# Optimization experiments

Measured on AMD Instinct MI355X. Metric: run time of the kernel, lower is better.

Reference implementation:

```python
import jax, jax.numpy as jnp
import numpy as np

T = 3000
D_MODEL = 1280
NUM_HEADS = 20
HEAD_DIM = D_MODEL // NUM_HEADS
N_CHUNKS = 4  # block-diagonal chunks of 750 frames each
NEG = -1e9


def _block_diag_mask(t, n_chunks):
    chunk = t // n_chunks
    seg = jnp.arange(t) // chunk  # [T]
    allow = seg[:, None] == seg[None, :]
    return jnp.where(allow, 0.0, NEG).astype(jnp.float32)


def setup_inputs() -> dict:
    key = jax.random.key(0)
    ks = jax.random.split(key, 9)
    s = 1.0 / np.sqrt(D_MODEL)
    inp = {
        "hidden_states": jax.random.normal(ks[0], (T, D_MODEL), jnp.float32),
        "attention_mask": _block_diag_mask(T, N_CHUNKS),
        "wq": jax.random.normal(ks[1], (D_MODEL, D_MODEL), jnp.float32) * s,
        "bq": jax.random.normal(ks[2], (D_MODEL,), jnp.float32) * 0.02,
        "wk": jax.random.normal(ks[3], (D_MODEL, D_MODEL), jnp.float32) * s,
        "bk": jax.random.normal(ks[4], (D_MODEL,), jnp.float32) * 0.02,
        "wv": jax.random.normal(ks[5], (D_MODEL, D_MODEL), jnp.float32) * s,
        "bv": jax.random.normal(ks[6], (D_MODEL,), jnp.float32) * 0.02,
        "wo": jax.random.normal(ks[7], (D_MODEL, D_MODEL), jnp.float32) * s,
        "bo": jax.random.normal(ks[8], (D_MODEL,), jnp.float32) * 0.02,
    }
    return inp


def reference(hidden_states, attention_mask, wq, bq, wk, bk, wv, bv, wo, bo):
    # hidden_states: [T, D], attention_mask: [T, T] additive (0 / -inf)
    t = hidden_states.shape[0]
    scaling = HEAD_DIM ** -0.5
    # projections -> [H, T, hd]  (weights stored as [in, out] = W^T of nn.Linear)
    q = (hidden_states @ wq + bq).reshape(t, NUM_HEADS, HEAD_DIM).transpose(1, 0, 2)
    k = (hidden_states @ wk + bk).reshape(t, NUM_HEADS, HEAD_DIM).transpose(1, 0, 2)
    v = (hidden_states @ wv + bv).reshape(t, NUM_HEADS, HEAD_DIM).transpose(1, 0, 2)
    # [H, T, T] scores + additive mask, fp32 softmax
    scores = jnp.einsum("htd,hsd->hts", q, k) * scaling + attention_mask[None]
    attn = jax.nn.softmax(scores.astype(jnp.float32), axis=-1).astype(q.dtype)
    out = jnp.einsum("hts,hsd->htd", attn, v)  # [H, T, hd]
    out = out.transpose(1, 0, 2).reshape(t, D_MODEL)
    return out @ wo + bo
```

## Files before the change

kernel.cpp:

```cpp
#include <hip/hip_runtime.h>

#define T_LEN 3000
#define DM 1280
#define NUM_HEADS 20
#define N_CH 4
#define CHUNK 750
#define CHUNK_PAD 768
#define T_PAD 3072

typedef __bf16 bf16x8 __attribute__((ext_vector_type(8)));
typedef float f32x4 __attribute__((ext_vector_type(4)));

typedef const __attribute__((address_space(1))) void* gas_p;
typedef __attribute__((address_space(3))) void* las_p;
#define GLOAD16(g, l) __builtin_amdgcn_global_load_lds((gas_p)(g), (las_p)(l), 16, 0, 0)

__device__ __forceinline__ unsigned short f2bf(float f) {
  union { float f; unsigned u; } x; x.f = f;
  unsigned r = x.u + 0x7FFFu + ((x.u >> 16) & 1u);
  return (unsigned short)(r >> 16);
}

__global__ __launch_bounds__(256) void cvt_bf16_kernel(
    const float* __restrict__ in, unsigned short* __restrict__ out) {
  int i = blockIdx.x * 256 + threadIdx.x;
  ushort4 o;
  if (i < T_LEN * DM / 4) {
    const float4 v = ((const float4*)in)[i];
    o.x = f2bf(v.x); o.y = f2bf(v.y); o.z = f2bf(v.z); o.w = f2bf(v.w);
  } else {
    o.x = 0; o.y = 0; o.z = 0; o.w = 0;
  }
  ((ushort4*)out)[i] = o;
}

__global__ __launch_bounds__(256) void tr_bf16_kernel(
    const float* __restrict__ w0, const float* __restrict__ w1,
    const float* __restrict__ w2, const float* __restrict__ w3,
    unsigned short* __restrict__ out) {
  const int z = blockIdx.z;
  const float* in = z == 0 ? w0 : (z == 1 ? w1 : (z == 2 ? w2 : w3));
  unsigned short* o = out + (size_t)z * DM * DM;
  __shared__ float tile[32][33];
  const int x = threadIdx.x, y0 = threadIdx.y;
  const int n0 = blockIdx.x * 32, k0 = blockIdx.y * 32;
  for (int y = y0; y < 32; y += 8) tile[y][x] = in[(k0 + y) * DM + n0 + x];
  __syncthreads();
  for (int y = y0; y < 32; y += 8) o[(n0 + y) * DM + k0 + x] = f2bf(tile[x][y]);
}

__global__ __launch_bounds__(256) void vpad_zero_kernel(unsigned short* __restrict__ Vtb) {
  int i = blockIdx.x * 256 + threadIdx.x;
  if (i >= NUM_HEADS * 64 * N_CH * (CHUNK_PAD - CHUNK)) return;
  int c = i % (CHUNK_PAD - CHUNK); int r = i / (CHUNK_PAD - CHUNK);
  int ch = r % N_CH; int row = r / N_CH;
  Vtb[(size_t)row * T_PAD + ch * CHUNK_PAD + CHUNK + c] = 0;
}

template <int MODE>
__global__ __launch_bounds__(256) void gemm_kernel(
    const unsigned short* __restrict__ A, const unsigned short* __restrict__ Bt,
    const float* __restrict__ b0, const float* __restrict__ b1, const float* __restrict__ b2,
    unsigned short* __restrict__ dq, unsigned short* __restrict__ dk,
    unsigned short* __restrict__ dv, float* __restrict__ df) {
  __shared__ unsigned short As[128][64];
  __shared__ unsigned short Bs[64][64];
  const int tid = threadIdx.x;
  const int lane = tid & 63, wave = tid >> 6;
  const int h = lane >> 4, lr = lane & 15;
  const int wm = wave >> 1, wn = wave & 1;
  const int t0 = blockIdx.x * 128, n0 = blockIdx.y * 64;
  const int rs = lane >> 3;
  const int c8 = (lane & 7) ^ rs;

  const unsigned short* Ab = A + (size_t)t0 * DM + c8 * 8;
  const unsigned short* Bb = Bt + (size_t)n0 * DM + c8 * 8;

  f32x4 acc[4][2];
  const f32x4 zero4 = {0.f, 0.f, 0.f, 0.f};
#pragma unroll
  for (int i = 0; i < 4; i++)
#pragma unroll
    for (int j = 0; j < 2; j++) acc[i][j] = zero4;

  const int NT = DM / 64;
  for (int kt = 0; kt < NT; ++kt) {
    const int k0 = kt * 64;
#pragma unroll
    for (int i = 0; i < 4; ++i) {
      const int blk = wave * 4 + i;
      GLOAD16(Ab + (size_t)(blk * 8 + rs) * DM + k0, &As[blk * 8][0]);
    }
#pragma unroll
    for (int i = 0; i < 2; ++i) {
      const int blk = wave * 2 + i;
      GLOAD16(Bb + (size_t)(blk * 8 + rs) * DM + k0, &Bs[blk * 8][0]);
    }
    __syncthreads();
#pragma unroll
    for (int kk = 0; kk < 2; ++kk) {
      bf16x8 a[4], b[2];
      const int csw = ((kk * 4 + h) ^ (lr & 7)) * 8;
#pragma unroll
      for (int mi = 0; mi < 4; mi++) a[mi] = *(const bf16x8*)&As[wm * 64 + mi * 16 + lr][csw];
#pragma unroll
      for (int ni = 0; ni < 2; ni++) b[ni] = *(const bf16x8*)&Bs[wn * 32 + ni * 16 + lr][csw];
#pragma unroll
      for (int mi = 0; mi < 4; mi++)
#pragma unroll
        for (int ni = 0; ni < 2; ni++)
          acc[mi][ni] = __builtin_amdgcn_mfma_f32_16x16x32_bf16(a[mi], b[ni], acc[mi][ni], 0, 0, 0);
    }
    __syncthreads();
  }

  const int sec = (MODE == 0) ? ((int)blockIdx.y / 20) : 0;
  const float* bias = (MODE == 0) ? (sec == 0 ? b0 : (sec == 1 ? b1 : b2)) : b0;
  const float qs = (MODE == 0 && sec == 0) ? 0.125f : 1.0f;
#pragma unroll
  for (int mi = 0; mi < 4; mi++) {
#pragma unroll
    for (int j = 0; j < 4; j++) {
      int t = t0 + wm * 64 + mi * 16 + h * 4 + j;
      if (t >= T_LEN) continue;
#pragma unroll
      for (int ni = 0; ni < 2; ni++) {
        int n = n0 + wn * 32 + ni * 16 + lr;
        if (MODE == 0) {
          int nn = n - sec * DM;
          float v = (acc[mi][ni][j] + bias[nn]) * qs;
          if (sec < 2) {
            unsigned short* dst = sec == 0 ? dq : dk;
            dst[(size_t)(nn >> 6) * (T_PAD * 64) + (size_t)t * 64 + (nn & 63)] = f2bf(v);
          } else {
            int ch = t / CHUNK, s = t - ch * CHUNK;
            dv[(size_t)(nn >> 6) * (64 * T_PAD) + (size_t)(nn & 63) * T_PAD + ch * CHUNK_PAD + s] = f2bf(v);
          }
        } else {
          df[(size_t)t * DM + n] = acc[mi][ni][j] + bias[n];
        }
      }
    }
  }
}

__global__ __launch_bounds__(256) void attn_kernel(
    const unsigned short* __restrict__ Qb, const unsigned short* __restrict__ Kb,
    const unsigned short* __restrict__ Vtb, unsigned short* __restrict__ Ctx) {
  __shared__ unsigned short Ks[2][64][64];
  __shared__ unsigned short Vs[2][64][64];
  __shared__ unsigned short Ps[4][16][64];
  const int tid = threadIdx.x;
  const int lane = tid & 63, wave = tid >> 6;
  const int h = lane >> 4, lr = lane & 15;
  const int rs = lane >> 3;
  const int c8 = (lane & 7) ^ rs;
  int bid = blockIdx.x;
  const int qt = bid % 12; bid /= 12;
  const int ch = bid % N_CH; bid /= N_CH;
  const int hh = bid;

  const unsigned short* Qh = Qb + (size_t)hh * (T_PAD * 64);
  const unsigned short* Kh = Kb + (size_t)hh * (T_PAD * 64) + (size_t)(ch * CHUNK) * 64 + c8 * 8;
  const unsigned short* Vh = Vtb + (size_t)hh * (64 * T_PAD) + ch * CHUNK_PAD + c8 * 8;

  const int qrow0 = qt * 64 + wave * 16;
  const int tq = ch * CHUNK + qrow0 + lr;
  bf16x8 aq[2];
#pragma unroll
  for (int kk = 0; kk < 2; kk++)
    aq[kk] = *(const bf16x8*)(Qh + (size_t)tq * 64 + kk * 32 + h * 8);

  const f32x4 zero4 = {0.f, 0.f, 0.f, 0.f};
  f32x4 oacc[4];
#pragma unroll
  for (int i = 0; i < 4; i++) oacc[i] = zero4;
  float l_part[4] = {0.f, 0.f, 0.f, 0.f};

#define A_STAGE(buf, kt) do {                                                   \
    const int s0_ = (kt) * 64;                                                  \
    _Pragma("unroll")                                                           \
    for (int i_ = 0; i_ < 2; ++i_) {                                            \
      const int blk_ = wave * 2 + i_;                                           \
      const int r_ = blk_ * 8 + rs;                                             \
      GLOAD16(Kh + (size_t)(s0_ + r_) * 64, &Ks[buf][blk_ * 8][0]);             \
      GLOAD16(Vh + (size_t)r_ * T_PAD + s0_, &Vs[buf][blk_ * 8][0]);            \
    } } while (0)

  A_STAGE(0, 0);
  __syncthreads();
  int cur = 0;
  for (int kt = 0; kt < 12; ++kt) {
    if (kt + 1 < 12) A_STAGE(cur ^ 1, kt + 1);

    f32x4 sacc[4];
#pragma unroll
    for (int i = 0; i < 4; i++) sacc[i] = zero4;
#pragma unroll
    for (int kk = 0; kk < 2; kk++) {
      const int csw = ((kk * 4 + h) ^ (lr & 7)) * 8;
      bf16x8 bk[4];
#pragma unroll
      for (int ni = 0; ni < 4; ni++) bk[ni] = *(const bf16x8*)&Ks[cur][ni * 16 + lr][csw];
#pragma unroll
      for (int ni = 0; ni < 4; ni++)
        sacc[ni] = __builtin_amdgcn_mfma_f32_16x16x32_bf16(aq[kk], bk[ni], sacc[ni], 0, 0, 0);
    }

    const bool last = (kt == 11);
    float pexp[4][4];
#pragma unroll
    for (int ni = 0; ni < 4; ni++) {
#pragma unroll
      for (int j = 0; j < 4; j++) {
        float e = __expf(sacc[ni][j]);
        if (last && (ni * 16 + lr >= CHUNK - 704)) e = 0.f;
        pexp[ni][j] = e;
        l_part[j] += e;
      }
    }

#pragma unroll
    for (int ni = 0; ni < 4; ni++) {
#pragma unroll
      for (int j = 0; j < 4; j++) {
        int row = h * 4 + j;
        int col = ni * 16 + lr;
        Ps[wave][row][((col >> 3) ^ (row & 7)) * 8 + (col & 7)] = f2bf(pexp[ni][j]);
      }
    }

#pragma unroll
    for (int kk = 0; kk < 2; kk++) {
      const int csw = ((kk * 4 + h) ^ (lr & 7)) * 8;
      bf16x8 ap = *(const bf16x8*)&Ps[wave][lr][csw];
      bf16x8 bv[4];
#pragma unroll
      for (int nd = 0; nd < 4; nd++) bv[nd] = *(const bf16x8*)&Vs[cur][nd * 16 + lr][csw];
#pragma unroll
      for (int nd = 0; nd < 4; nd++)
        oacc[nd] = __builtin_amdgcn_mfma_f32_16x16x32_bf16(ap, bv[nd], oacc[nd], 0, 0, 0);
    }
    __syncthreads();
    cur ^= 1;
  }
#undef A_STAGE

#pragma unroll
  for (int j = 0; j < 4; j++) {
    float l = l_part[j];
#pragma unroll
    for (int off = 1; off < 16; off <<= 1) l += __shfl_xor(l, off, 64);
    int qr = qrow0 + h * 4 + j;
    if (qr >= CHUNK) continue;
    int t = ch * CHUNK + qr;
    float inv = 1.f / l;
#pragma unroll
    for (int nd = 0; nd < 4; nd++) {
      int d = nd * 16 + lr;
      Ctx[(size_t)t * DM + hh * 64 + d] = f2bf(oacc[nd][j] * inv);
    }
  }
}

extern "C" void kernel_launch(void* const* d_in, const int* in_sizes, int n_in,
                              void* d_out, int out_size, void* d_ws, size_t ws_size,
                              hipStream_t stream) {
  const float* hs = (const float*)d_in[0];
  const float* wq = (const float*)d_in[2];
  const float* bq = (const float*)d_in[3];
  const float* wk = (const float*)d_in[4];
  const float* bk = (const float*)d_in[5];
  const float* wv = (const float*)d_in[6];
  const float* bv = (const float*)d_in[7];
  const float* wo = (const float*)d_in[8];
  const float* bo = (const float*)d_in[9];

  char* ws = (char*)d_ws;
  unsigned short* Xb = (unsigned short*)ws;   ws += (size_t)T_PAD * DM * 2;
  unsigned short* Wcat = (unsigned short*)ws; ws += (size_t)4 * DM * DM * 2;
  unsigned short* Qb = (unsigned short*)ws;   ws += (size_t)NUM_HEADS * T_PAD * 64 * 2;
  unsigned short* Kb = (unsigned short*)ws;   ws += (size_t)NUM_HEADS * T_PAD * 64 * 2;
  unsigned short* Vtb = (unsigned short*)ws;  ws += (size_t)NUM_HEADS * 64 * T_PAD * 2;
  unsigned short* Ctx = (unsigned short*)ws;  ws += (size_t)T_PAD * DM * 2;

  cvt_bf16_kernel<<<T_PAD * DM / 4 / 256, 256, 0, stream>>>(hs, Xb);
  tr_bf16_kernel<<<dim3(40, 40, 4), dim3(32, 8), 0, stream>>>(wq, wk, wv, wo, Wcat);
  vpad_zero_kernel<<<(NUM_HEADS * 64 * N_CH * (CHUNK_PAD - CHUNK) + 255) / 256, 256, 0, stream>>>(Vtb);

  gemm_kernel<0><<<dim3(24, 60), 256, 0, stream>>>(Xb, Wcat, bq, bk, bv, Qb, Kb, Vtb, nullptr);

  attn_kernel<<<NUM_HEADS * N_CH * 12, 256, 0, stream>>>(Qb, Kb, Vtb, Ctx);

  gemm_kernel<1><<<dim3(24, 20), 256, 0, stream>>>(Ctx, Wcat + (size_t)3 * DM * DM, bo, nullptr, nullptr,
                                                   nullptr, nullptr, nullptr, (float*)d_out);
}
```

Baseline: 129.3 us.

## Use 256x256 double-buffered pipelined GEMM for fused QKV projection

Replaces the 128x64-tile QKV projection GEMM with a dedicated 512-thread kernel using 256x256 tiles. It double-buffers LDS with async global-to-LDS loads interleaved across eight compute phases, and raises MFMA wave priority while computing. The aim is more operand reuse per byte loaded and overlap of memory traffic with matrix math. The trade-off is only 180 blocks (fewer than the CU count), 128 KB of LDS per block, and heavy register use from 32 accumulators. The output projection keeps the old kernel, split into its own non-templated version.

```diff
diff --git a/kernel.cpp b/kernel.cpp
--- a/kernel.cpp
+++ b/kernel.cpp
@@ -57,12 +57,128 @@
   Vtb[(size_t)row * T_PAD + ch * CHUNK_PAD + CHUNK + c] = 0;
 }
 
-template <int MODE>
-__global__ __launch_bounds__(256) void gemm_kernel(
+__global__ __launch_bounds__(512, 2) void gemm256_kernel(
     const unsigned short* __restrict__ A, const unsigned short* __restrict__ Bt,
     const float* __restrict__ b0, const float* __restrict__ b1, const float* __restrict__ b2,
     unsigned short* __restrict__ dq, unsigned short* __restrict__ dk,
-    unsigned short* __restrict__ dv, float* __restrict__ df) {
+    unsigned short* __restrict__ dv) {
+  __shared__ unsigned short Asd[2][256][64];
+  __shared__ unsigned short Bsd[2][256][64];
+  const int tid = threadIdx.x;
+  const int lane = tid & 63, wave = tid >> 6;
+  const int h = lane >> 4, lr = lane & 15;
+  const int wm = wave >> 2, wn = wave & 3;
+  const int t0 = blockIdx.x * 256, n0 = blockIdx.y * 256;
+
+  const int r8 = lane >> 3;
+  const int sg = (lane & 7) ^ r8;
+  const unsigned short* Ast = A + (size_t)(t0 + wave * 8 + r8) * DM + sg * 8;
+  const unsigned short* Bst = Bt + (size_t)(n0 + wave * 8 + r8) * DM + sg * 8;
+
+#define STG_A(BUF, HALF, KT) do {                                                        \
+    GLOAD16(Ast + (size_t)((HALF) * 128) * DM + (size_t)(KT) * 64,                       \
+            &Asd[BUF][(HALF) * 128 + wave * 8][0]);                                      \
+    GLOAD16(Ast + (size_t)((HALF) * 128 + 64) * DM + (size_t)(KT) * 64,                  \
+            &Asd[BUF][(HALF) * 128 + 64 + wave * 8][0]);                                 \
+  } while (0)
+#define STG_B(BUF, HALF, KT) do {                                                        \
+    GLOAD16(Bst + (size_t)((HALF) * 128) * DM + (size_t)(KT) * 64,                       \
+            &Bsd[BUF][(HALF) * 128 + wave * 8][0]);                                      \
+    GLOAD16(Bst + (size_t)((HALF) * 128 + 64) * DM + (size_t)(KT) * 64,                  \
+            &Bsd[BUF][(HALF) * 128 + 64 + wave * 8][0]);                                 \
+  } while (0)
+
+  f32x4 acc[8][4];
+  const f32x4 zero4 = {0.f, 0.f, 0.f, 0.f};
+#pragma unroll
+  for (int i = 0; i < 8; i++)
+#pragma unroll
+    for (int j = 0; j < 4; j++) acc[i][j] = zero4;
+
+#define PHASE(BUF, MH, NH, STAGE_STMT, GATE_STMT) do {                                   \
+    bf16x8 pa[4][2], pb[2][2];                                                           \
+    _Pragma("unroll") for (int mf = 0; mf < 4; mf++)                                     \
+      _Pragma("unroll") for (int kk = 0; kk < 2; kk++) {                                 \
+        const int R = (MH) * 128 + wm * 64 + mf * 16 + lr;                               \
+        pa[mf][kk] = *(const bf16x8*)&Asd[BUF][R][((kk * 4 + h) ^ (lr & 7)) * 8];        \
+      }                                                                                  \
+    _Pragma("unroll") for (int nf = 0; nf < 2; nf++)                                     \
+      _Pragma("unroll") for (int kk = 0; kk < 2; kk++) {                                 \
+        const int Cc = (NH) * 128 + wn * 32 + nf * 16 + lr;                              \
+        pb[nf][kk] = *(const bf16x8*)&Bsd[BUF][Cc][((kk * 4 + h) ^ (lr & 7)) * 8];       \
+      }                                                                                  \
+    STAGE_STMT;                                                                          \
+    __builtin_amdgcn_s_barrier();                                                        \
+    __builtin_amdgcn_s_setprio(1);                                                       \
+    _Pragma("unroll") for (int mf = 0; mf < 4; mf++)                                     \
+      _Pragma("unroll") for (int nf = 0; nf < 2; nf++)                                   \
+        _Pragma("unroll") for (int kk = 0; kk < 2; kk++)                                 \
+          acc[(MH) * 4 + mf][(NH) * 2 + nf] = __builtin_amdgcn_mfma_f32_16x16x32_bf16(   \
+              pa[mf][kk], pb[nf][kk], acc[(MH) * 4 + mf][(NH) * 2 + nf], 0, 0, 0);       \
+    __builtin_amdgcn_s_setprio(0);                                                       \
+    GATE_STMT;                                                                           \
+    __builtin_amdgcn_s_barrier();                                                        \
+  } while (0)
+
+  STG_A(0, 0, 0); STG_B(0, 0, 0); STG_A(0, 1, 0); STG_B(0, 1, 0);
+  STG_A(1, 0, 1); STG_B(1, 0, 1);
+  asm volatile("s_waitcnt vmcnt(4)" ::: "memory");
+  __builtin_amdgcn_s_barrier();
+
+#pragma unroll 1
+  for (int i = 0; i < 10; ++i) {
+    const int tA = 2 * i, tB = 2 * i + 1;
+    PHASE(0, 0, 0, STG_A(1, 1, tB), );
+    PHASE(0, 0, 1, STG_B(1, 1, tB), );
+    PHASE(0, 1, 0, if (i < 9) STG_A(0, 0, tA + 2), );
+    PHASE(0, 1, 1, if (i < 9) STG_B(0, 0, tA + 2),
+          if (i < 9) { asm volatile("s_waitcnt vmcnt(4)" ::: "memory"); }
+          else       { asm volatile("s_waitcnt vmcnt(0)" ::: "memory"); });
+    PHASE(1, 0, 0, if (i < 9) STG_A(0, 1, tA + 2), );
+    PHASE(1, 0, 1, if (i < 9) STG_B(0, 1, tA + 2), );
+    PHASE(1, 1, 0, if (i < 9) STG_A(1, 0, tB + 2), );
+    PHASE(1, 1, 1, if (i < 9) STG_B(1, 0, tB + 2),
+          if (i < 9) { asm volatile("s_waitcnt vmcnt(4)" ::: "memory"); });
+  }
+#undef PHASE
+#undef STG_A
+#undef STG_B
+
+  const int sec = (int)blockIdx.y / 5;
+  const float* bias = sec == 0 ? b0 : (sec == 1 ? b1 : b2);
+  const float qs = sec == 0 ? 0.125f : 1.0f;
+#pragma unroll
+  for (int mh = 0; mh < 2; mh++) {
+#pragma unroll
+    for (int mf = 0; mf < 4; mf++) {
+#pragma unroll
+      for (int jj = 0; jj < 4; jj++) {
+        int t = t0 + mh * 128 + wm * 64 + mf * 16 + h * 4 + jj;
+        if (t >= T_LEN) continue;
+#pragma unroll
+        for (int nh = 0; nh < 2; nh++) {
+#pragma unroll
+          for (int nf = 0; nf < 2; nf++) {
+            int n = n0 + nh * 128 + wn * 32 + nf * 16 + lr;
+            int nn = n - sec * DM;
+            float v = (acc[mh * 4 + mf][nh * 2 + nf][jj] + bias[nn]) * qs;
+            if (sec < 2) {
+              unsigned short* dst = sec == 0 ? dq : dk;
+              dst[(size_t)(nn >> 6) * (T_PAD * 64) + (size_t)t * 64 + (nn & 63)] = f2bf(v);
+            } else {
+              int ch = t / CHUNK, s = t - ch * CHUNK;
+              dv[(size_t)(nn >> 6) * (64 * T_PAD) + (size_t)(nn & 63) * T_PAD + ch * CHUNK_PAD + s] = f2bf(v);
+            }
+          }
+        }
+      }
+    }
+  }
+}
+
+__global__ __launch_bounds__(256) void gemm_out_kernel(
+    const unsigned short* __restrict__ A, const unsigned short* __restrict__ Bt,
+    const float* __restrict__ b0, float* __restrict__ df) {
   __shared__ unsigned short As[128][64];
   __shared__ unsigned short Bs[64][64];
   const int tid = threadIdx.x;
@@ -114,9 +230,6 @@
     __syncthreads();
   }
 
-  const int sec = (MODE == 0) ? ((int)blockIdx.y / 20) : 0;
-  const float* bias = (MODE == 0) ? (sec == 0 ? b0 : (sec == 1 ? b1 : b2)) : b0;
-  const float qs = (MODE == 0 && sec == 0) ? 0.125f : 1.0f;
 #pragma unroll
   for (int mi = 0; mi < 4; mi++) {
 #pragma unroll
@@ -126,19 +239,7 @@
 #pragma unroll
       for (int ni = 0; ni < 2; ni++) {
         int n = n0 + wn * 32 + ni * 16 + lr;
-        if (MODE == 0) {
-          int nn = n - sec * DM;
-          float v = (acc[mi][ni][j] + bias[nn]) * qs;
-          if (sec < 2) {
-            unsigned short* dst = sec == 0 ? dq : dk;
-            dst[(size_t)(nn >> 6) * (T_PAD * 64) + (size_t)t * 64 + (nn & 63)] = f2bf(v);
-          } else {
-            int ch = t / CHUNK, s = t - ch * CHUNK;
-            dv[(size_t)(nn >> 6) * (64 * T_PAD) + (size_t)(nn & 63) * T_PAD + ch * CHUNK_PAD + s] = f2bf(v);
-          }
-        } else {
-          df[(size_t)t * DM + n] = acc[mi][ni][j] + bias[n];
-        }
+        df[(size_t)t * DM + n] = acc[mi][ni][j] + b0[n];
       }
     }
   }
@@ -288,10 +389,9 @@
   tr_bf16_kernel<<<dim3(40, 40, 4), dim3(32, 8), 0, stream>>>(wq, wk, wv, wo, Wcat);
   vpad_zero_kernel<<<(NUM_HEADS * 64 * N_CH * (CHUNK_PAD - CHUNK) + 255) / 256, 256, 0, stream>>>(Vtb);
 
-  gemm_kernel<0><<<dim3(24, 60), 256, 0, stream>>>(Xb, Wcat, bq, bk, bv, Qb, Kb, Vtb, nullptr);
+  gemm256_kernel<<<dim3(12, 15), 512, 0, stream>>>(Xb, Wcat, bq, bk, bv, Qb, Kb, Vtb);
 
   attn_kernel<<<NUM_HEADS * N_CH * 12, 256, 0, stream>>>(Qb, Kb, Vtb, Ctx);
 
-  gemm_kernel<1><<<dim3(24, 20), 256, 0, stream>>>(Ctx, Wcat + (size_t)3 * DM * DM, bo, nullptr, nullptr,
-                                                   nullptr, nullptr, nullptr, (float*)d_out);
-}
+  gemm_out_kernel<<<dim3(24, 20), 256, 0, stream>>>(Ctx, Wcat + (size_t)3 * DM * DM, bo, (float*)d_out);
+}
```

New measurement: 159.0 us. 1.23x slower.

## Merge prep kernels into one launch and widen QKV GEMM tile to 128x128

Applied to the files above, without the earlier changes.

The three preprocessing kernels (input bf16 conversion, weight transpose, V padding zeroing) are folded into one launch that dispatches on block index. The QKV projection GEMM gets its own kernel with a 128x128 output tile (4x4 MFMA tiles per wave), which halves the number of blocks and raises reuse of each loaded A tile. This cuts launch overhead and global traffic for the largest GEMM, but the wider tile uses more registers and LDS, which may lower occupancy. The single zeroing block is now serial, though its work is small.

```diff
diff --git a/kernel.cpp b/kernel.cpp
--- a/kernel.cpp
+++ b/kernel.cpp
@@ -21,48 +21,130 @@
   return (unsigned short)(r >> 16);
 }
 
-__global__ __launch_bounds__(256) void cvt_bf16_kernel(
-    const float* __restrict__ in, unsigned short* __restrict__ out) {
-  int i = blockIdx.x * 256 + threadIdx.x;
-  ushort4 o;
-  if (i < T_LEN * DM / 4) {
-    const float4 v = ((const float4*)in)[i];
-    o.x = f2bf(v.x); o.y = f2bf(v.y); o.z = f2bf(v.z); o.w = f2bf(v.w);
-  } else {
-    o.x = 0; o.y = 0; o.z = 0; o.w = 0;
-  }
-  ((ushort4*)out)[i] = o;
-}
-
-__global__ __launch_bounds__(256) void tr_bf16_kernel(
+#define NB_CVT (T_PAD * DM / 4 / 256)
+#define NB_TR  (40 * 40 * 4)
+__global__ __launch_bounds__(256) void prep_kernel(
+    const float* __restrict__ hs, unsigned short* __restrict__ Xb,
     const float* __restrict__ w0, const float* __restrict__ w1,
     const float* __restrict__ w2, const float* __restrict__ w3,
-    unsigned short* __restrict__ out) {
-  const int z = blockIdx.z;
-  const float* in = z == 0 ? w0 : (z == 1 ? w1 : (z == 2 ? w2 : w3));
-  unsigned short* o = out + (size_t)z * DM * DM;
-  __shared__ float tile[32][33];
-  const int x = threadIdx.x, y0 = threadIdx.y;
-  const int n0 = blockIdx.x * 32, k0 = blockIdx.y * 32;
-  for (int y = y0; y < 32; y += 8) tile[y][x] = in[(k0 + y) * DM + n0 + x];
-  __syncthreads();
-  for (int y = y0; y < 32; y += 8) o[(n0 + y) * DM + k0 + x] = f2bf(tile[x][y]);
-}
-
-__global__ __launch_bounds__(256) void vpad_zero_kernel(unsigned short* __restrict__ Vtb) {
-  int i = blockIdx.x * 256 + threadIdx.x;
-  if (i >= NUM_HEADS * 64 * N_CH * (CHUNK_PAD - CHUNK)) return;
-  int c = i % (CHUNK_PAD - CHUNK); int r = i / (CHUNK_PAD - CHUNK);
-  int ch = r % N_CH; int row = r / N_CH;
-  Vtb[(size_t)row * T_PAD + ch * CHUNK_PAD + CHUNK + c] = 0;
-}
-
-template <int MODE>
-__global__ __launch_bounds__(256) void gemm_kernel(
+    unsigned short* __restrict__ Wcat, unsigned short* __restrict__ Vtb) {
+  const int b = blockIdx.x;
+  if (b < NB_CVT) {
+    int i = b * 256 + threadIdx.x;
+    ushort4 o;
+    if (i < T_LEN * DM / 4) {
+      const float4 v = ((const float4*)hs)[i];
+      o.x = f2bf(v.x); o.y = f2bf(v.y); o.z = f2bf(v.z); o.w = f2bf(v.w);
+    } else {
+      o.x = 0; o.y = 0; o.z = 0; o.w = 0;
+    }
+    ((ushort4*)Xb)[i] = o;
+    return;
+  }
+  if (b < NB_CVT + NB_TR) {
+    const int bb = b - NB_CVT;
+    const int z = bb / 1600;
+    const int rem = bb - z * 1600;
+    const int bx = rem % 40, by = rem / 40;
+    const float* in = z == 0 ? w0 : (z == 1 ? w1 : (z == 2 ? w2 : w3));
+    unsigned short* o = Wcat + (size_t)z * DM * DM;
+    __shared__ float tile[32][33];
+    const int x = threadIdx.x & 31, y0 = threadIdx.x >> 5;
+    const int n0 = bx * 32, k0 = by * 32;
+    for (int y = y0; y < 32; y += 8) tile[y][x] = in[(k0 + y) * DM + n0 + x];
+    __syncthreads();
+    for (int y = y0; y < 32; y += 8) o[(n0 + y) * DM + k0 + x] = f2bf(tile[x][y]);
+    return;
+  }
+  for (int i = threadIdx.x; i < NUM_HEADS * 64 * N_CH * (CHUNK_PAD - CHUNK); i += 256) {
+    int c = i % (CHUNK_PAD - CHUNK); int r = i / (CHUNK_PAD - CHUNK);
+    int ch = r % N_CH; int row = r / N_CH;
+    Vtb[(size_t)row * T_PAD + ch * CHUNK_PAD + CHUNK + c] = 0;
+  }
+}
+
+__global__ __launch_bounds__(256) void gemm_qkv_kernel(
     const unsigned short* __restrict__ A, const unsigned short* __restrict__ Bt,
     const float* __restrict__ b0, const float* __restrict__ b1, const float* __restrict__ b2,
     unsigned short* __restrict__ dq, unsigned short* __restrict__ dk,
-    unsigned short* __restrict__ dv, float* __restrict__ df) {
+    unsigned short* __restrict__ dv) {
+  __shared__ unsigned short As[128][64];
+  __shared__ unsigned short Bs[128][64];
+  const int tid = threadIdx.x;
+  const int lane = tid & 63, wave = tid >> 6;
+  const int h = lane >> 4, lr = lane & 15;
+  const int wm = wave >> 1, wn = wave & 1;
+  const int t0 = blockIdx.x * 128, n0 = blockIdx.y * 128;
+  const int rs = lane >> 3;
+  const int c8 = (lane & 7) ^ rs;
+
+  const unsigned short* Ab = A + (size_t)t0 * DM + c8 * 8;
+  const unsigned short* Bb = Bt + (size_t)n0 * DM + c8 * 8;
+
+  f32x4 acc[4][4];
+  const f32x4 zero4 = {0.f, 0.f, 0.f, 0.f};
+#pragma unroll
+  for (int i = 0; i < 4; i++)
+#pragma unroll
+    for (int j = 0; j < 4; j++) acc[i][j] = zero4;
+
+  const int NT = DM / 64;
+  for (int kt = 0; kt < NT; ++kt) {
+    const int k0 = kt * 64;
+#pragma unroll
+    for (int i = 0; i < 4; ++i) {
+      const int blk = wave * 4 + i;
+      const size_t ro = (size_t)(blk * 8 + rs) * DM + k0;
+      GLOAD16(Ab + ro, &As[blk * 8][0]);
+      GLOAD16(Bb + ro, &Bs[blk * 8][0]);
+    }
+    __syncthreads();
+#pragma unroll
+    for (int kk = 0; kk < 2; ++kk) {
+      bf16x8 a[4], b[4];
+      const int csw = ((kk * 4 + h) ^ (lr & 7)) * 8;
+#pragma unroll
+      for (int mi = 0; mi < 4; mi++) a[mi] = *(const bf16x8*)&As[wm * 64 + mi * 16 + lr][csw];
+#pragma unroll
+      for (int ni = 0; ni < 4; ni++) b[ni] = *(const bf16x8*)&Bs[wn * 64 + ni * 16 + lr][csw];
+#pragma unroll
+      for (int mi = 0; mi < 4; mi++)
+#pragma unroll
+        for (int ni = 0; ni < 4; ni++)
+          acc[mi][ni] = __builtin_amdgcn_mfma_f32_16x16x32_bf16(a[mi], b[ni], acc[mi][ni], 0, 0, 0);
+    }
+    __syncthreads();
+  }
+
+  const int sec = (int)blockIdx.y / 10;
+  const float* bias = sec == 0 ? b0 : (sec == 1 ? b1 : b2);
+  const float qs = sec == 0 ? 0.125f : 1.0f;
+#pragma unroll
+  for (int mi = 0; mi < 4; mi++) {
+#pragma unroll
+    for (int j = 0; j < 4; j++) {
+      int t = t0 + wm * 64 + mi * 16 + h * 4 + j;
+      if (t >= T_LEN) continue;
+#pragma unroll
+      for (int ni = 0; ni < 4; ni++) {
+        int n = n0 + wn * 64 + ni * 16 + lr;
+        int nn = n - sec * DM;
+        float v = (acc[mi][ni][j] + bias[nn]) * qs;
+        if (sec < 2) {
+          unsigned short* dst = sec == 0 ? dq : dk;
+          dst[(size_t)(nn >> 6) * (T_PAD * 64) + (size_t)t * 64 + (nn & 63)] = f2bf(v);
+        } else {
+          int ch = t / CHUNK, s = t - ch * CHUNK;
+          dv[(size_t)(nn >> 6) * (64 * T_PAD) + (size_t)(nn & 63) * T_PAD + ch * CHUNK_PAD + s] = f2bf(v);
+        }
+      }
+    }
+  }
+}
+
+__global__ __launch_bounds__(256) void gemm_out_kernel(
+    const unsigned short* __restrict__ A, const unsigned short* __restrict__ Bt,
+    const float* __restrict__ b0, float* __restrict__ df) {
   __shared__ unsigned short As[128][64];
   __shared__ unsigned short Bs[64][64];
   const int tid = threadIdx.x;
@@ -114,9 +196,6 @@
     __syncthreads();
   }
 
-  const int sec = (MODE == 0) ? ((int)blockIdx.y / 20) : 0;
-  const float* bias = (MODE == 0) ? (sec == 0 ? b0 : (sec == 1 ? b1 : b2)) : b0;
-  const float qs = (MODE == 0 && sec == 0) ? 0.125f : 1.0f;
 #pragma unroll
   for (int mi = 0; mi < 4; mi++) {
 #pragma unroll
@@ -126,19 +205,7 @@
 #pragma unroll
       for (int ni = 0; ni < 2; ni++) {
         int n = n0 + wn * 32 + ni * 16 + lr;
-        if (MODE == 0) {
-          int nn = n - sec * DM;
-          float v = (acc[mi][ni][j] + bias[nn]) * qs;
-          if (sec < 2) {
-            unsigned short* dst = sec == 0 ? dq : dk;
-            dst[(size_t)(nn >> 6) * (T_PAD * 64) + (size_t)t * 64 + (nn & 63)] = f2bf(v);
-          } else {
-            int ch = t / CHUNK, s = t - ch * CHUNK;
-            dv[(size_t)(nn >> 6) * (64 * T_PAD) + (size_t)(nn & 63) * T_PAD + ch * CHUNK_PAD + s] = f2bf(v);
-          }
-        } else {
-          df[(size_t)t * DM + n] = acc[mi][ni][j] + bias[n];
-        }
+        df[(size_t)t * DM + n] = acc[mi][ni][j] + b0[n];
       }
     }
   }
@@ -284,14 +351,11 @@
   unsigned short* Vtb = (unsigned short*)ws;  ws += (size_t)NUM_HEADS * 64 * T_PAD * 2;
   unsigned short* Ctx = (unsigned short*)ws;  ws += (size_t)T_PAD * DM * 2;
 
-  cvt_bf16_kernel<<<T_PAD * DM / 4 / 256, 256, 0, stream>>>(hs, Xb);
-  tr_bf16_kernel<<<dim3(40, 40, 4), dim3(32, 8), 0, stream>>>(wq, wk, wv, wo, Wcat);
-  vpad_zero_kernel<<<(NUM_HEADS * 64 * N_CH * (CHUNK_PAD - CHUNK) + 255) / 256, 256, 0, stream>>>(Vtb);
-
-  gemm_kernel<0><<<dim3(24, 60), 256, 0, stream>>>(Xb, Wcat, bq, bk, bv, Qb, Kb, Vtb, nullptr);
+  prep_kernel<<<NB_CVT + NB_TR + 1, 256, 0, stream>>>(hs, Xb, wq, wk, wv, wo, Wcat, Vtb);
+
+  gemm_qkv_kernel<<<dim3(24, 30), 256, 0, stream>>>(Xb, Wcat, bq, bk, bv, Qb, Kb, Vtb);
 
   attn_kernel<<<NUM_HEADS * N_CH * 12, 256, 0, stream>>>(Qb, Kb, Vtb, Ctx);
 
-  gemm_kernel<1><<<dim3(24, 20), 256, 0, stream>>>(Ctx, Wcat + (size_t)3 * DM * DM, bo, nullptr, nullptr,
-                                                   nullptr, nullptr, nullptr, (float*)d_out);
-}
+  gemm_out_kernel<<<dim3(24, 20), 256, 0, stream>>>(Ctx, Wcat + (size_t)3 * DM * DM, bo, (float*)d_out);
+}
```

Result: no change. 130.6 us (+1.0%).
